# Optimization experiments

Measured on AMD Instinct MI355X. Metric: run time of the kernel, lower is better.

Reference implementation:

```python
import jax, jax.numpy as jnp
import numpy as np

C = 1024
RANK = 8


def _layernorm(x, g, b, eps=1e-5):
    mu = jnp.mean(x, axis=-1, keepdims=True)
    var = jnp.var(x, axis=-1, keepdims=True)
    return (x - mu) * jax.lax.rsqrt(var + eps) * g + b


def setup_inputs() -> dict:
    key = jax.random.key(0)
    ks = jax.random.split(key, 10)
    B, T = 4, 4096
    x = jax.random.normal(ks[0], (B, T, C), dtype=jnp.float32)
    # parameters (match torch inits)
    W0 = jnp.eye(C, dtype=jnp.float32) * 0.1
    A_init = jax.random.normal(ks[1], (C, RANK), dtype=jnp.float32) * 0.01
    B_init = jnp.zeros((RANK, C), dtype=jnp.float32)
    log_lr = jnp.full((C,), float(np.log(0.1)), dtype=jnp.float32)
    s = 1.0 / np.sqrt(C)
    Wq = jax.random.uniform(ks[2], (C, C), minval=-s, maxval=s, dtype=jnp.float32)
    Wk = jax.random.uniform(ks[3], (C, C), minval=-s, maxval=s, dtype=jnp.float32)
    Wv = jax.random.uniform(ks[4], (C, C), minval=-s, maxval=s, dtype=jnp.float32)
    Wo = jax.random.uniform(ks[5], (C, C), minval=-s, maxval=s, dtype=jnp.float32)
    Wg = jax.random.uniform(ks[6], (C, C), minval=-s, maxval=s, dtype=jnp.float32)
    ln_g = jnp.ones((C,), dtype=jnp.float32)
    ln_b = jnp.zeros((C,), dtype=jnp.float32)
    ls_g = jnp.full((C,), 1e-4, dtype=jnp.float32)  # LayerScale gamma
    return {"x": x, "W0": W0, "A_init": A_init, "B_init": B_init,
            "log_lr": log_lr, "Wq": Wq, "Wk": Wk, "Wv": Wv, "Wo": Wo,
            "Wg": Wg, "ln_g": ln_g, "ln_b": ln_b, "ls_g": ls_g}


def reference(x, W0, A_init, B_init, log_lr, Wq, Wk, Wv, Wo, Wg, ln_g, ln_b, ls_g):
    B, T, _ = x.shape
    h = _layernorm(x, ln_g, ln_b)
    # dual-form TTT (training path: q/k/v projections, full K @ W0)
    Q = jnp.einsum('btc,dc->btd', h, Wq)
    K = jnp.einsum('btc,dc->btd', h, Wk)
    V = jnp.einsum('btc,dc->btd', h, Wv)
    lr = jnp.minimum(jnp.exp(log_lr), 1.0)  # clamp(max=1.0)
    y0 = jnp.einsum('btc,cd->btd', K, W0) + jnp.einsum('btr,rd->btd', jnp.einsum('btc,cr->btr', K, A_init), B_init)
    error = y0 - V
    loss = jnp.mean(error ** 2)
    gradient = K * error                     # [B,T,C]
    grad_cumsum = jnp.cumsum(gradient, axis=1)
    grad_shift = jnp.concatenate([jnp.zeros((B, 1, gradient.shape[-1]), gradient.dtype), grad_cumsum[:, :-1, :]], axis=1)
    correction = Q * lr[None, None, :] * grad_shift
    pos = jnp.arange(1, T + 1, dtype=correction.dtype)
    pos_scale = (1.0 / (1.0 + 0.1 * jnp.log(pos)))[None, :, None]
    out = y0 - correction * pos_scale
    # gate, out projection, layer scale, residual
    gate = jax.nn.sigmoid(jnp.einsum('btc,dc->btd', x, Wg))
    out = out * gate
    out = jnp.einsum('btc,dc->btd', out, Wo) * ls_g
    return (x + out, loss)
```

## Files before the change

### kernel.cpp

```cpp
#include <hip/hip_runtime.h>
#include <stdint.h>
#include <math.h>

typedef unsigned short u16;
typedef __attribute__((ext_vector_type(8))) short short8;
typedef __attribute__((ext_vector_type(4))) float f32x4;

__device__ __forceinline__ float bf2f(u16 u){
  union { unsigned int i; float f; } v; v.i = ((unsigned int)u) << 16; return v.f;
}
__device__ __forceinline__ u16 f2bf(float f){
  union { float f; unsigned int i; } v; v.f = f;
  return (u16)((v.i + 0x7FFFu + ((v.i >> 16) & 1u)) >> 16);
}

__global__ void ln_prep(const float* __restrict__ x, const float* __restrict__ g,
                        const float* __restrict__ bta, u16* __restrict__ h,
                        u16* __restrict__ xb, float* __restrict__ loss){
  int tid = threadIdx.x, wid = tid >> 6, lane = tid & 63;
  if (blockIdx.x == 0 && tid == 0) loss[0] = 0.f;
  int row = blockIdx.x * 4 + wid;
  const float4* xr = (const float4*)(x + (size_t)row * 1024);
  float4 v[4]; float s = 0.f, s2 = 0.f;
  #pragma unroll
  for (int i = 0; i < 4; ++i){
    v[i] = xr[i*64 + lane];
    s  += v[i].x + v[i].y + v[i].z + v[i].w;
    s2 += v[i].x*v[i].x + v[i].y*v[i].y + v[i].z*v[i].z + v[i].w*v[i].w;
  }
  #pragma unroll
  for (int o = 1; o < 64; o <<= 1){ s += __shfl_xor(s, o); s2 += __shfl_xor(s2, o); }
  float mu   = s * (1.0f/1024.0f);
  float var  = s2 * (1.0f/1024.0f) - mu*mu;
  float rstd = rsqrtf(var + 1e-5f);
  #pragma unroll
  for (int i = 0; i < 4; ++i){
    float4 gg = ((const float4*)g)[i*64 + lane];
    float4 bb = ((const float4*)bta)[i*64 + lane];
    ushort4 hv, xv;
    hv.x = f2bf((v[i].x-mu)*rstd*gg.x + bb.x);
    hv.y = f2bf((v[i].y-mu)*rstd*gg.y + bb.y);
    hv.z = f2bf((v[i].z-mu)*rstd*gg.z + bb.z);
    hv.w = f2bf((v[i].w-mu)*rstd*gg.w + bb.w);
    xv.x = f2bf(v[i].x); xv.y = f2bf(v[i].y); xv.z = f2bf(v[i].z); xv.w = f2bf(v[i].w);
    ((ushort4*)h )[(size_t)row*256 + i*64 + lane] = hv;
    ((ushort4*)xb)[(size_t)row*256 + i*64 + lane] = xv;
  }
}

__global__ void conv5(const float* __restrict__ a, const float* __restrict__ b,
                      const float* __restrict__ c, const float* __restrict__ d,
                      const float* __restrict__ e,
                      const float* __restrict__ W0, const float* __restrict__ Ai,
                      const float* __restrict__ Bi,
                      u16* oa, u16* ob, u16* oc, u16* od, u16* oe,
                      u16* __restrict__ Wet){
  __shared__ float tile[32][33];
  int sel = blockIdx.y;
  int tid = threadIdx.x;
  if (sel == 5){
    int d0 = (blockIdx.x & 31)*32, e0 = (blockIdx.x >> 5)*32;
    int lr = tid >> 5, lc = tid & 31;
    #pragma unroll
    for (int s = 0; s < 4; ++s){
      int ee = e0 + s*8 + lr, dd = d0 + lc;
      float v = W0[(size_t)ee*1024 + dd];
      #pragma unroll
      for (int r = 0; r < 8; ++r) v += Ai[ee*8 + r] * Bi[(size_t)r*1024 + dd];
      tile[s*8 + lr][lc] = v;
    }
    __syncthreads();
    #pragma unroll
    for (int s = 0; s < 4; ++s){
      int dd = d0 + s*8 + lr, ee = e0 + lc;
      Wet[(size_t)dd*1024 + ee] = f2bf(tile[lc][s*8 + lr]);
    }
    return;
  }
  const float* s = sel==0?a : sel==1?b : sel==2?c : sel==3?d : e;
  u16* o = sel==0?oa : sel==1?ob : sel==2?oc : sel==3?od : oe;
  int i = blockIdx.x*256 + tid;
  float4 v = ((const float4*)s)[i];
  ushort4 r; r.x=f2bf(v.x); r.y=f2bf(v.y); r.z=f2bf(v.z); r.w=f2bf(v.w);
  ((ushort4*)o)[i] = r;
}

#define VMW(N)  asm volatile("s_waitcnt vmcnt(" #N ")" ::: "memory")
#define SBAR    __builtin_amdgcn_s_barrier()
#define SCHED0  __builtin_amdgcn_sched_barrier(0)

template<int EPI>
__device__ __forceinline__ void gemm256_body(const u16* __restrict__ A, const u16* __restrict__ Bm,
    u16* __restrict__ Cb, float* __restrict__ Cf, const float* __restrict__ lsg,
    const float* __restrict__ xres, int mblk, int nblk)
{
  __shared__ u16 As[4][8192];
  __shared__ u16 Bs[4][8192];
  const int tid  = threadIdx.x;
  const int lane = tid & 63;
  const int w    = tid >> 6;
  const int wm = w >> 2, wn = w & 3;
  const int l15 = lane & 15, quad = lane >> 4;
  const int m0 = mblk * 256, n0 = nblk * 256;

  const int sl   = (lane & 7) ^ (lane >> 3);
  const int srow = 2*(w*8 + (lane >> 3)) + (sl >> 2);
  const int scol = (sl & 3) * 8;
  const u16* gA = A  + (size_t)(m0 + srow)*1024 + scol;
  const u16* gB = Bm + (size_t)(n0 + srow)*1024 + scol;
  const int ldsOff = w * 512;

  const int phys8 = (((((l15 & 1) << 2) | quad) ^ (l15 >> 1))) * 8;
  const int rdA = (wm*64 + (l15 >> 1))*64 + phys8;
  const int rdB = (wn*32 + (l15 >> 1))*64 + phys8;

  f32x4 acc[8][4] = {};

#define SA(T) do{ const int _ss=(T)&3; const size_t _k=(size_t)(T)*32; \
    __builtin_amdgcn_global_load_lds((const __attribute__((address_space(1))) unsigned int*)(gA + _k), \
        (__attribute__((address_space(3))) unsigned int*)(&As[_ss][ldsOff]), 16, 0, 0); \
    __builtin_amdgcn_global_load_lds((const __attribute__((address_space(1))) unsigned int*)(gA + _k + 131072), \
        (__attribute__((address_space(3))) unsigned int*)(&As[_ss][ldsOff + 4096]), 16, 0, 0); \
  }while(0)
#define SB(T) do{ const int _ss=(T)&3; const size_t _k=(size_t)(T)*32; \
    __builtin_amdgcn_global_load_lds((const __attribute__((address_space(1))) unsigned int*)(gB + _k), \
        (__attribute__((address_space(3))) unsigned int*)(&Bs[_ss][ldsOff]), 16, 0, 0); \
    __builtin_amdgcn_global_load_lds((const __attribute__((address_space(1))) unsigned int*)(gB + _k + 131072), \
        (__attribute__((address_space(3))) unsigned int*)(&Bs[_ss][ldsOff + 4096]), 16, 0, 0); \
  }while(0)

#define SLICE(T, VMOP, DS) do{ \
    VMOP; \
    SCHED0; SBAR; SCHED0; \
    if (DS){ SA((T)+3); SB((T)+3); } \
    const int _s = (T) & 3; \
    const u16* _as = &As[_s][0]; \
    const u16* _bs = &Bs[_s][0]; \
    short8 afv[8], bfv[4]; \
    _Pragma("unroll") \
    for (int _j = 0; _j < 4; ++_j) bfv[_j] = *(const short8*)(_bs + rdB + _j*512); \
    _Pragma("unroll") \
    for (int _i = 0; _i < 8; ++_i) afv[_i] = *(const short8*)(_as + rdA + _i*512); \
    _Pragma("unroll") \
    for (int _i = 0; _i < 8; ++_i){ \
      _Pragma("unroll") \
      for (int _j = 0; _j < 4; ++_j) \
        acc[_i][_j] = __builtin_amdgcn_mfma_f32_16x16x32_bf16(afv[_i], bfv[_j], acc[_i][_j], 0, 0, 0); \
    } \
  }while(0)

  SA(0); SB(0); SA(1); SB(1); SA(2); SB(2);

  #pragma unroll 1
  for (int t = 0; t < 28; t += 4){
    SLICE(t+0, VMW(8), 1);
    SLICE(t+1, VMW(8), 1);
    SLICE(t+2, VMW(8), 1);
    SLICE(t+3, VMW(8), 1);
  }
  SLICE(28, VMW(8), 1);
  SLICE(29, VMW(8), 0);
  SLICE(30, VMW(4), 0);
  SLICE(31, VMW(0), 0);
#undef SLICE
#undef SA
#undef SB

  const int rbase = quad * 4;
  if (EPI == 0){
    #pragma unroll
    for (int i = 0; i < 8; ++i){
      int row = m0 + wm*128 + i*16 + rbase;
      #pragma unroll
      for (int j = 0; j < 4; ++j){
        int col = n0 + wn*64 + j*16 + l15;
        #pragma unroll
        for (int r = 0; r < 4; ++r)
          Cb[(size_t)(row + r)*1024 + col] = f2bf(acc[i][j][r]);
      }
    }
  } else {
    float lsv[4];
    #pragma unroll
    for (int j = 0; j < 4; ++j) lsv[j] = lsg[n0 + wn*64 + j*16 + l15];
    #pragma unroll
    for (int i = 0; i < 8; ++i){
      int row = m0 + wm*128 + i*16 + rbase;
      #pragma unroll
      for (int j = 0; j < 4; ++j){
        int col = n0 + wn*64 + j*16 + l15;
        #pragma unroll
        for (int r = 0; r < 4; ++r){
          size_t idx = (size_t)(row + r)*1024 + col;
          Cf[idx] = acc[i][j][r] * lsv[j] + xres[idx];
        }
      }
    }
  }
}

__global__ __launch_bounds__(512, 2) void gemm_qkvg(
    const u16* __restrict__ h, const u16* __restrict__ xb,
    const u16* __restrict__ Wqb, const u16* __restrict__ Wkb,
    const u16* __restrict__ Wvb, const u16* __restrict__ Wgb,
    u16* __restrict__ Qb, u16* __restrict__ Kb,
    u16* __restrict__ Vb, u16* __restrict__ Gb){
  int bid = blockIdx.x;
  int swz = (bid & 7) * 128 + (bid >> 3);
  int mblk = swz >> 4;
  int rem  = swz & 15;
  int sel  = rem >> 2, nblk = rem & 3;
  const u16* A  = (sel == 3) ? xb : h;
  const u16* Bm = sel==0?Wqb : sel==1?Wkb : sel==2?Wvb : Wgb;
  u16* Out      = sel==0?Qb  : sel==1?Kb  : sel==2?Vb  : Gb;
  gemm256_body<0>(A, Bm, Out, nullptr, nullptr, nullptr, mblk, nblk);
}

__global__ __launch_bounds__(512, 2) void gemm_plain(
    const u16* __restrict__ A, const u16* __restrict__ Bm, u16* __restrict__ C){
  int bid = blockIdx.x;
  int swz = (bid & 7) * 32 + (bid >> 3);
  gemm256_body<0>(A, Bm, C, nullptr, nullptr, nullptr, swz >> 2, swz & 3);
}

__global__ __launch_bounds__(512, 2) void gemm_final(
    const u16* __restrict__ A, const u16* __restrict__ Bm,
    float* __restrict__ C, const float* __restrict__ lsg,
    const float* __restrict__ xres, const float* __restrict__ loss){
  if (blockIdx.x == 0 && threadIdx.x == 0)
    C[16777216] = loss[0] * (1.0f/16777216.0f);
  int bid = blockIdx.x;
  int swz = (bid & 7) * 32 + (bid >> 3);
  gemm256_body<1>(A, Bm, nullptr, C, lsg, xres, swz >> 2, swz & 3);
}

__global__ __launch_bounds__(256) void scan1(
    const u16* __restrict__ Kb, const u16* __restrict__ Vb,
    const u16* __restrict__ Yb, float* __restrict__ part,
    float* __restrict__ loss){
  int tid = threadIdx.x;
  int c4 = tid * 4;
  int ch = blockIdx.x, b = blockIdx.y;
  size_t base = ((size_t)b*4096 + (size_t)ch*32)*1024 + c4;
  float g0=0.f,g1=0.f,g2=0.f,g3=0.f, ls=0.f;
  #pragma unroll 8
  for (int t = 0; t < 32; ++t){
    size_t idx = base + (size_t)t*1024;
    ushort4 k4 = *(const ushort4*)(Kb + idx);
    ushort4 v4 = *(const ushort4*)(Vb + idx);
    ushort4 y4 = *(const ushort4*)(Yb + idx);
    float e;
    e = bf2f(y4.x)-bf2f(v4.x); g0 += bf2f(k4.x)*e; ls += e*e;
    e = bf2f(y4.y)-bf2f(v4.y); g1 += bf2f(k4.y)*e; ls += e*e;
    e = bf2f(y4.z)-bf2f(v4.z); g2 += bf2f(k4.z)*e; ls += e*e;
    e = bf2f(y4.w)-bf2f(v4.w); g3 += bf2f(k4.w)*e; ls += e*e;
  }
  float4 gv; gv.x=g0; gv.y=g1; gv.z=g2; gv.w=g3;
  *(float4*)(part + (size_t)(b*128 + ch)*1024 + c4) = gv;
  #pragma unroll
  for (int o = 32; o > 0; o >>= 1) ls += __shfl_down(ls, o);
  __shared__ float red[4];
  if ((tid & 63) == 0) red[tid >> 6] = ls;
  __syncthreads();
  if (tid == 0) atomicAdd(loss, red[0]+red[1]+red[2]+red[3]);
}

__global__ __launch_bounds__(256) void scan2(
    const u16* __restrict__ Kb, const u16* __restrict__ Vb,
    const u16* __restrict__ Yb, const u16* __restrict__ Qb,
    const u16* __restrict__ Gb, const float* __restrict__ part,
    const float* __restrict__ llr, u16* __restrict__ OutPre){
  int tid = threadIdx.x;
  int c4 = tid * 4;
  int ch = blockIdx.x, b = blockIdx.y;
  float r0=0.f,r1=0.f,r2=0.f,r3=0.f;
  for (int j = 0; j < ch; ++j){
    float4 p = *(const float4*)(part + (size_t)(b*128 + j)*1024 + c4);
    r0 += p.x; r1 += p.y; r2 += p.z; r3 += p.w;
  }
  float4 ll = *(const float4*)(llr + c4);
  float lr0 = fminf(__expf(ll.x), 1.0f);
  float lr1 = fminf(__expf(ll.y), 1.0f);
  float lr2 = fminf(__expf(ll.z), 1.0f);
  float lr3 = fminf(__expf(ll.w), 1.0f);
  size_t base = ((size_t)b*4096 + (size_t)ch*32)*1024 + c4;
  #pragma unroll 4
  for (int t = 0; t < 32; ++t){
    size_t idx = base + (size_t)t*1024;
    ushort4 k4 = *(const ushort4*)(Kb + idx);
    ushort4 v4 = *(const ushort4*)(Vb + idx);
    ushort4 y4 = *(const ushort4*)(Yb + idx);
    ushort4 q4 = *(const ushort4*)(Qb + idx);
    ushort4 g4 = *(const ushort4*)(Gb + idx);
    float ps = 1.0f/(1.0f + 0.1f*__logf((float)(ch*32 + t + 1)));
    ushort4 ov;
    float e, gate, o;
    e = bf2f(y4.x)-bf2f(v4.x); gate = 1.0f/(1.0f + __expf(-bf2f(g4.x)));
    o = (bf2f(y4.x) - bf2f(q4.x)*lr0*r0*ps) * gate; ov.x = f2bf(o); r0 += bf2f(k4.x)*e;
    e = bf2f(y4.y)-bf2f(v4.y); gate = 1.0f/(1.0f + __expf(-bf2f(g4.y)));
    o = (bf2f(y4.y) - bf2f(q4.y)*lr1*r1*ps) * gate; ov.y = f2bf(o); r1 += bf2f(k4.y)*e;
    e = bf2f(y4.z)-bf2f(v4.z); gate = 1.0f/(1.0f + __expf(-bf2f(g4.z)));
    o = (bf2f(y4.z) - bf2f(q4.z)*lr2*r2*ps) * gate; ov.z = f2bf(o); r2 += bf2f(k4.z)*e;
    e = bf2f(y4.w)-bf2f(v4.w); gate = 1.0f/(1.0f + __expf(-bf2f(g4.w)));
    o = (bf2f(y4.w) - bf2f(q4.w)*lr3*r3*ps) * gate; ov.w = f2bf(o); r3 += bf2f(k4.w)*e;
    *(ushort4*)(OutPre + idx) = ov;
  }
}

extern "C" void kernel_launch(void* const* d_in, const int* in_sizes, int n_in,
                              void* d_out, int out_size, void* d_ws, size_t ws_size,
                              hipStream_t stream){
  const float* x   = (const float*)d_in[0];
  const float* W0  = (const float*)d_in[1];
  const float* Ai  = (const float*)d_in[2];
  const float* Bi  = (const float*)d_in[3];
  const float* llr = (const float*)d_in[4];
  const float* Wq  = (const float*)d_in[5];
  const float* Wk  = (const float*)d_in[6];
  const float* Wv  = (const float*)d_in[7];
  const float* Wo  = (const float*)d_in[8];
  const float* Wg  = (const float*)d_in[9];
  const float* lng = (const float*)d_in[10];
  const float* lnb = (const float*)d_in[11];
  const float* lsg = (const float*)d_in[12];
  float* out = (float*)d_out;

  const size_t TOK = 16384, CC = 1024;
  char* p = (char*)d_ws;
  float* loss = (float*)p; p += 256;
  u16* h   = (u16*)p; p += TOK*CC*2;
  u16* xb  = (u16*)p; p += TOK*CC*2;
  u16* Qb  = (u16*)p; p += TOK*CC*2;
  u16* Kb  = (u16*)p; p += TOK*CC*2;
  u16* Vb  = (u16*)p; p += TOK*CC*2;
  u16* Gb  = (u16*)p; p += TOK*CC*2;
  u16* Wqb = (u16*)p; p += CC*CC*2;
  u16* Wkb = (u16*)p; p += CC*CC*2;
  u16* Wvb = (u16*)p; p += CC*CC*2;
  u16* Wgb = (u16*)p; p += CC*CC*2;
  u16* Wob = (u16*)p; p += CC*CC*2;
  u16* Wet = (u16*)p; p += CC*CC*2;
  float* part = (float*)p; p += (size_t)4*128*1024*4;

  ln_prep<<<4096, 256, 0, stream>>>(x, lng, lnb, h, xb, loss);
  conv5<<<dim3(1024, 6), 256, 0, stream>>>(Wq, Wk, Wv, Wg, Wo, W0, Ai, Bi,
                                           Wqb, Wkb, Wvb, Wgb, Wob, Wet);
  gemm_qkvg<<<1024, 512, 0, stream>>>(h, xb, Wqb, Wkb, Wvb, Wgb, Qb, Kb, Vb, Gb);
  gemm_plain<<<256, 512, 0, stream>>>(Kb, Wet, h);
  scan1<<<dim3(128, 4), 256, 0, stream>>>(Kb, Vb, h, part, loss);
  scan2<<<dim3(128, 4), 256, 0, stream>>>(Kb, Vb, h, Qb, Gb, part, llr, Qb);
  gemm_final<<<256, 512, 0, stream>>>(Qb, Wob, out, lsg, x, loss);
}
```

Before: 460.2 us.

## Restructure scan kernels to one channel per thread with longer time chunks

Changes the two cumulative-sum scan kernels from 4 channels per thread with 32-step chunks (128 chunks) to 1 channel per thread with 128-step chunks (32 chunks), using a 3D grid split over channel blocks. This shrinks the partial-sum buffer and the serial prefix loop over previous chunks, while keeping the same number of blocks. In exchange, each thread now does scalar 2-byte loads instead of 8-byte vector loads, and each thread's serial time loop is four times longer. It also switches __expf/__logf to the precise expf/logf.

```diff
diff --git a/kernel.cpp b/kernel.cpp
--- a/kernel.cpp
+++ b/kernel.cpp
@@ -234,29 +234,22 @@
   gemm256_body<1>(A, Bm, nullptr, C, lsg, xres, swz >> 2, swz & 3);
 }
 
-__global__ __launch_bounds__(256) void scan1(
-    const u16* __restrict__ Kb, const u16* __restrict__ Vb,
-    const u16* __restrict__ Yb, float* __restrict__ part,
-    float* __restrict__ loss){
+__global__ void scan1(const u16* __restrict__ Kb, const u16* __restrict__ Vb,
+                      const u16* __restrict__ Yb, float* __restrict__ part,
+                      float* __restrict__ loss){
   int tid = threadIdx.x;
-  int c4 = tid * 4;
-  int ch = blockIdx.x, b = blockIdx.y;
-  size_t base = ((size_t)b*4096 + (size_t)ch*32)*1024 + c4;
-  float g0=0.f,g1=0.f,g2=0.f,g3=0.f, ls=0.f;
+  int c = blockIdx.x*256 + tid;
+  int ch = blockIdx.y, b = blockIdx.z;
+  size_t base = ((size_t)b*4096 + (size_t)ch*128)*1024 + c;
+  float g = 0.f, ls = 0.f;
   #pragma unroll 8
-  for (int t = 0; t < 32; ++t){
+  for (int t = 0; t < 128; ++t){
     size_t idx = base + (size_t)t*1024;
-    ushort4 k4 = *(const ushort4*)(Kb + idx);
-    ushort4 v4 = *(const ushort4*)(Vb + idx);
-    ushort4 y4 = *(const ushort4*)(Yb + idx);
-    float e;
-    e = bf2f(y4.x)-bf2f(v4.x); g0 += bf2f(k4.x)*e; ls += e*e;
-    e = bf2f(y4.y)-bf2f(v4.y); g1 += bf2f(k4.y)*e; ls += e*e;
-    e = bf2f(y4.z)-bf2f(v4.z); g2 += bf2f(k4.z)*e; ls += e*e;
-    e = bf2f(y4.w)-bf2f(v4.w); g3 += bf2f(k4.w)*e; ls += e*e;
-  }
-  float4 gv; gv.x=g0; gv.y=g1; gv.z=g2; gv.w=g3;
-  *(float4*)(part + (size_t)(b*128 + ch)*1024 + c4) = gv;
+    float kv = bf2f(Kb[idx]), vv = bf2f(Vb[idx]), yv = bf2f(Yb[idx]);
+    float e = yv - vv;
+    g += kv*e; ls += e*e;
+  }
+  part[((size_t)(b*32 + ch))*1024 + c] = g;
   #pragma unroll
   for (int o = 32; o > 0; o >>= 1) ls += __shfl_down(ls, o);
   __shared__ float red[4];
@@ -265,45 +258,29 @@
   if (tid == 0) atomicAdd(loss, red[0]+red[1]+red[2]+red[3]);
 }
 
-__global__ __launch_bounds__(256) void scan2(
-    const u16* __restrict__ Kb, const u16* __restrict__ Vb,
-    const u16* __restrict__ Yb, const u16* __restrict__ Qb,
-    const u16* __restrict__ Gb, const float* __restrict__ part,
-    const float* __restrict__ llr, u16* __restrict__ OutPre){
+__global__ void scan2(const u16* __restrict__ Kb, const u16* __restrict__ Vb,
+                      const u16* __restrict__ Yb, const u16* __restrict__ Qb,
+                      const u16* __restrict__ Gb, const float* __restrict__ part,
+                      const float* __restrict__ llr, u16* __restrict__ OutPre){
   int tid = threadIdx.x;
-  int c4 = tid * 4;
-  int ch = blockIdx.x, b = blockIdx.y;
-  float r0=0.f,r1=0.f,r2=0.f,r3=0.f;
-  for (int j = 0; j < ch; ++j){
-    float4 p = *(const float4*)(part + (size_t)(b*128 + j)*1024 + c4);
-    r0 += p.x; r1 += p.y; r2 += p.z; r3 += p.w;
-  }
-  float4 ll = *(const float4*)(llr + c4);
-  float lr0 = fminf(__expf(ll.x), 1.0f);
-  float lr1 = fminf(__expf(ll.y), 1.0f);
-  float lr2 = fminf(__expf(ll.z), 1.0f);
-  float lr3 = fminf(__expf(ll.w), 1.0f);
-  size_t base = ((size_t)b*4096 + (size_t)ch*32)*1024 + c4;
+  int c = blockIdx.x*256 + tid;
+  int ch = blockIdx.y, b = blockIdx.z;
+  float run = 0.f;
+  for (int j = 0; j < ch; ++j) run += part[((size_t)(b*32 + j))*1024 + c];
+  float lrc = fminf(expf(llr[c]), 1.0f);
+  size_t base = ((size_t)b*4096 + (size_t)ch*128)*1024 + c;
   #pragma unroll 4
-  for (int t = 0; t < 32; ++t){
+  for (int t = 0; t < 128; ++t){
     size_t idx = base + (size_t)t*1024;
-    ushort4 k4 = *(const ushort4*)(Kb + idx);
-    ushort4 v4 = *(const ushort4*)(Vb + idx);
-    ushort4 y4 = *(const ushort4*)(Yb + idx);
-    ushort4 q4 = *(const ushort4*)(Qb + idx);
-    ushort4 g4 = *(const ushort4*)(Gb + idx);
-    float ps = 1.0f/(1.0f + 0.1f*__logf((float)(ch*32 + t + 1)));
-    ushort4 ov;
-    float e, gate, o;
-    e = bf2f(y4.x)-bf2f(v4.x); gate = 1.0f/(1.0f + __expf(-bf2f(g4.x)));
-    o = (bf2f(y4.x) - bf2f(q4.x)*lr0*r0*ps) * gate; ov.x = f2bf(o); r0 += bf2f(k4.x)*e;
-    e = bf2f(y4.y)-bf2f(v4.y); gate = 1.0f/(1.0f + __expf(-bf2f(g4.y)));
-    o = (bf2f(y4.y) - bf2f(q4.y)*lr1*r1*ps) * gate; ov.y = f2bf(o); r1 += bf2f(k4.y)*e;
-    e = bf2f(y4.z)-bf2f(v4.z); gate = 1.0f/(1.0f + __expf(-bf2f(g4.z)));
-    o = (bf2f(y4.z) - bf2f(q4.z)*lr2*r2*ps) * gate; ov.z = f2bf(o); r2 += bf2f(k4.z)*e;
-    e = bf2f(y4.w)-bf2f(v4.w); gate = 1.0f/(1.0f + __expf(-bf2f(g4.w)));
-    o = (bf2f(y4.w) - bf2f(q4.w)*lr3*r3*ps) * gate; ov.w = f2bf(o); r3 += bf2f(k4.w)*e;
-    *(ushort4*)(OutPre + idx) = ov;
+    float kv = bf2f(Kb[idx]), vv = bf2f(Vb[idx]), yv = bf2f(Yb[idx]);
+    float qv = bf2f(Qb[idx]), gl = bf2f(Gb[idx]);
+    float e = yv - vv;
+    int tg = ch*128 + t + 1;
+    float ps = 1.0f/(1.0f + 0.1f*logf((float)tg));
+    float gate = 1.0f/(1.0f + expf(-gl));
+    float o = (yv - qv*lrc*run*ps) * gate;
+    OutPre[idx] = f2bf(o);
+    run += kv*e;
   }
 }
 
@@ -340,14 +317,14 @@
   u16* Wgb = (u16*)p; p += CC*CC*2;
   u16* Wob = (u16*)p; p += CC*CC*2;
   u16* Wet = (u16*)p; p += CC*CC*2;
-  float* part = (float*)p; p += (size_t)4*128*1024*4;
+  float* part = (float*)p; p += (size_t)4*32*1024*4;
 
   ln_prep<<<4096, 256, 0, stream>>>(x, lng, lnb, h, xb, loss);
   conv5<<<dim3(1024, 6), 256, 0, stream>>>(Wq, Wk, Wv, Wg, Wo, W0, Ai, Bi,
                                            Wqb, Wkb, Wvb, Wgb, Wob, Wet);
   gemm_qkvg<<<1024, 512, 0, stream>>>(h, xb, Wqb, Wkb, Wvb, Wgb, Qb, Kb, Vb, Gb);
   gemm_plain<<<256, 512, 0, stream>>>(Kb, Wet, h);
-  scan1<<<dim3(128, 4), 256, 0, stream>>>(Kb, Vb, h, part, loss);
-  scan2<<<dim3(128, 4), 256, 0, stream>>>(Kb, Vb, h, Qb, Gb, part, llr, Qb);
+  scan1<<<dim3(4, 32, 4), 256, 0, stream>>>(Kb, Vb, h, part, loss);
+  scan2<<<dim3(4, 32, 4), 256, 0, stream>>>(Kb, Vb, h, Qb, Gb, part, llr, Qb);
   gemm_final<<<256, 512, 0, stream>>>(Qb, Wob, out, lsg, x, loss);
 }
```

After: 446.6 us. -3.0%, faster.
